# Performance work log

Measured on AMD Instinct MI355X. Metric: run time of the kernel, lower is better.

The kernel has to match this reference:

```python
import jax, jax.numpy as jnp
from jax import lax
import numpy as np

N_CLASS = 11
ROI_SIZE = 7
SPATIAL_SCALE = 1.0 / 16.0
IMG_H, IMG_W = 600, 800
SCALE = 1.0
NMS_THRESH = 0.3
SCORE_THRESH = 0.05
LOC_MEAN = (0.0, 0.0, 0.0, 0.0)
LOC_STD = (0.1, 0.1, 0.2, 0.2)


def setup_inputs() -> dict:
    key = jax.random.key(0)
    ks = jax.random.split(key, 8)
    R = 512
    h = jax.random.normal(ks[0], (1, 512, 37, 50), dtype=jnp.float32)
    u = jax.random.uniform(ks[1], (R, 4), dtype=jnp.float32)
    y1 = u[:, 0] * (IMG_H - 64.0)
    x1 = u[:, 1] * (IMG_W - 64.0)
    y2 = y1 + 32.0 + u[:, 2] * (IMG_H - y1 - 32.0)
    x2 = x1 + 32.0 + u[:, 3] * (IMG_W - x1 - 32.0)
    rois = jnp.stack([y1, x1, y2, x2], axis=1)  # (ymin,xmin,ymax,xmax)
    roi_indices = jnp.zeros((R,), dtype=jnp.int32)
    W1 = jax.random.normal(ks[2], (25088, 4096), dtype=jnp.float32) * 0.01
    b1 = jnp.zeros((4096,), dtype=jnp.float32)
    W2 = jax.random.normal(ks[3], (4096, 4096), dtype=jnp.float32) * 0.01
    b2 = jnp.zeros((4096,), dtype=jnp.float32)
    Wloc = jax.random.normal(ks[4], (4096, N_CLASS * 4), dtype=jnp.float32) * 0.001
    bloc = jnp.zeros((N_CLASS * 4,), dtype=jnp.float32)
    Wscore = jax.random.normal(ks[5], (4096, N_CLASS), dtype=jnp.float32) * 0.01
    bscore = jnp.zeros((N_CLASS,), dtype=jnp.float32)
    return {"h": h, "rois": rois, "roi_indices": roi_indices, "W1": W1, "b1": b1,
            "W2": W2, "b2": b2, "Wloc": Wloc, "bloc": bloc, "Wscore": Wscore, "bscore": bscore}


def roi_pool(feat_all, rois_xyxy, roi_indices):
    # torchvision RoIPool: quantize coords by spatial_scale (round), +1 width, floor/ceil bins, max pool
    Hf, Wf = feat_all.shape[2], feat_all.shape[3]
    ys = jnp.arange(Hf)
    xs = jnp.arange(Wf)
    pb = jnp.arange(ROI_SIZE, dtype=jnp.float32)
    neg = jnp.array(-jnp.inf, feat_all.dtype)

    def one(args):
        roi, b = args
        x1, y1, x2, y2 = roi[0], roi[1], roi[2], roi[3]
        sw = jnp.round(x1 * SPATIAL_SCALE)
        ew = jnp.round(x2 * SPATIAL_SCALE)
        sh = jnp.round(y1 * SPATIAL_SCALE)
        eh = jnp.round(y2 * SPATIAL_SCALE)
        rw = jnp.maximum(ew - sw + 1.0, 1.0)
        rh = jnp.maximum(eh - sh + 1.0, 1.0)
        hstart = jnp.clip(jnp.floor(pb * rh / ROI_SIZE) + sh, 0, Hf)
        hend = jnp.clip(jnp.ceil((pb + 1.0) * rh / ROI_SIZE) + sh, 0, Hf)
        wstart = jnp.clip(jnp.floor(pb * rw / ROI_SIZE) + sw, 0, Wf)
        wend = jnp.clip(jnp.ceil((pb + 1.0) * rw / ROI_SIZE) + sw, 0, Wf)
        mh = (ys[None, :] >= hstart[:, None]) & (ys[None, :] < hend[:, None])  # [7,Hf]
        mw = (xs[None, :] >= wstart[:, None]) & (xs[None, :] < wend[:, None])  # [7,Wf]
        feat = jnp.take(feat_all, b, axis=0)  # [C,Hf,Wf]
        rowmax = jnp.where(mh[:, None, :, None], feat[None], neg).max(axis=2)  # [7ph,C,Wf]
        binmax = jnp.where(mw[:, None, None, :], rowmax[None], neg).max(axis=3)  # [7pw,7ph,C]
        pooled = jnp.transpose(binmax, (2, 1, 0))  # [C,ph,pw]
        empty = (hend <= hstart)[:, None] | (wend <= wstart)[None, :]  # [ph,pw]
        return jnp.where(empty[None], jnp.zeros((), feat.dtype), pooled)

    return lax.map(one, (rois_xyxy, roi_indices))  # [R,C,7,7]


def loc2bbox(src, loc):
    sh = src[:, 2] - src[:, 0]
    sw = src[:, 3] - src[:, 1]
    cy = src[:, 0] + 0.5 * sh
    cx = src[:, 1] + 0.5 * sw
    ncy = loc[:, 0] * sh + cy
    ncx = loc[:, 1] * sw + cx
    nh = jnp.exp(loc[:, 2]) * sh
    nw = jnp.exp(loc[:, 3]) * sw
    return jnp.stack([ncy - 0.5 * nh, ncx - 0.5 * nw, ncy + 0.5 * nh, ncx + 0.5 * nw], axis=1)


def _forward(h, rois, roi_indices, W1, b1, W2, b2, Wloc, bloc, Wscore, bscore):
    R = rois.shape[0]
    rois_xyxy = rois[:, jnp.array([1, 0, 3, 2])]  # (x1,y1,x2,y2) for RoIPool
    pool = roi_pool(h, rois_xyxy, roi_indices).reshape(R, -1)  # [R,25088]
    fc = jax.nn.relu(pool @ W1 + b1)
    fc7 = jax.nn.relu(fc @ W2 + b2)
    roi_cls_loc = fc7 @ Wloc + bloc  # [R,44]
    roi_scores = fc7 @ Wscore + bscore  # [R,11]
    mean = jnp.tile(jnp.asarray(LOC_MEAN, jnp.float32), N_CLASS)
    std = jnp.tile(jnp.asarray(LOC_STD, jnp.float32), N_CLASS)
    roi_cls_loc = roi_cls_loc * std + mean
    roi_s = rois / SCALE
    loc3 = roi_cls_loc.reshape(-1, N_CLASS, 4)
    roi3 = jnp.broadcast_to(roi_s[:, None, :], loc3.shape)
    cls_bbox = loc2bbox(roi3.reshape(-1, 4), loc3.reshape(-1, 4)).reshape(-1, N_CLASS * 4)
    cls_bbox = cls_bbox.at[:, 0::2].set(jnp.clip(cls_bbox[:, 0::2], 0.0, IMG_H))
    cls_bbox = cls_bbox.at[:, 1::2].set(jnp.clip(cls_bbox[:, 1::2], 0.0, IMG_W))
    prob = jax.nn.softmax(roi_scores, axis=1)
    return cls_bbox, prob


def _box_iou(a, b):  # yxyx, torchvision convention (no +1)
    tl = jnp.maximum(a[:, None, :2], b[None, :, :2])
    br = jnp.minimum(a[:, None, 2:], b[None, :, 2:])
    wh = jnp.clip(br - tl, 0.0)
    inter = wh[..., 0] * wh[..., 1]
    area_a = (a[:, 2] - a[:, 0]) * (a[:, 3] - a[:, 1])
    area_b = (b[:, 2] - b[:, 0]) * (b[:, 3] - b[:, 1])
    return inter / (area_a[:, None] + area_b[None, :] - inter)


def _nms_one(boxes, scores):
    R = scores.shape[0]
    valid = scores > SCORE_THRESH
    order = jnp.argsort(jnp.where(valid, -scores, jnp.inf))
    b = boxes[order]
    v = valid[order]
    iou = _box_iou(b, b)  # [R,R]
    idx = jnp.arange(R)

    def body(i, keep):
        suppress = keep[i] & (iou[i] > NMS_THRESH) & (idx > i)
        return keep & ~suppress

    keep = lax.fori_loop(0, R, body, v)
    return jnp.zeros((R,), bool).at[order].set(keep)


def reference(h, rois, roi_indices, W1, b1, W2, b2, Wloc, bloc, Wscore, bscore):
    cls_bbox, prob = _forward(h, rois, roi_indices, W1, b1, W2, b2, Wloc, bloc, Wscore, bscore)
    R = cls_bbox.shape[0]
    boxes_c = jnp.transpose(cls_bbox.reshape(R, N_CLASS, 4)[:, 1:], (1, 0, 2))  # [10,R,4]
    scores_c = prob[:, 1:].T  # [10,R]
    keep = jax.vmap(_nms_one)(boxes_c, scores_c)  # [10,R] bool per-class keep mask
    return cls_bbox, prob, keep
```

## Files before the change

### kernel.cpp

```cpp
#include <hip/hip_runtime.h>
#include <cfloat>
#include <cmath>
#include <stdint.h>

#define R_ROIS 512
#define NCLS 11
#define FEAT_C 512
#define FEAT_H 37
#define FEAT_W 50
#define POOLSZ 7
#define POOL_DIM (FEAT_C * POOLSZ * POOLSZ)
#define FC_DIM 4096
#define IMG_Hf 600.0f
#define IMG_Wf 800.0f
#define SPATIAL_SCALE 0.0625f
#define NMS_THR 0.3f
#define SCORE_THR 0.05f

#define OUT_PROB_OFF (R_ROIS * NCLS * 4)
#define OUT_KEEP_OFF (OUT_PROB_OFF + R_ROIS * NCLS)

typedef __bf16 bf16;
typedef __attribute__((ext_vector_type(8))) __bf16 v8bf;
typedef __attribute__((ext_vector_type(4))) __bf16 v4bf;
typedef __attribute__((ext_vector_type(4))) float f32x4;
typedef unsigned int u32;

__device__ __forceinline__ void gload_lds16(const void* g, void* l) {
  __builtin_amdgcn_global_load_lds(
      (const __attribute__((address_space(1))) u32*)(uintptr_t)g,
      (__attribute__((address_space(3))) u32*)(uintptr_t)l, 16, 0, 0);
}

__global__ __launch_bounds__(256) void roi_pool_kernel(
    const float* __restrict__ feat, const float* __restrict__ rois,
    const int* __restrict__ roi_idx, bf16* __restrict__ pool) {
  int r = blockIdx.x;
  float y1 = rois[r * 4 + 0], x1 = rois[r * 4 + 1];
  float y2 = rois[r * 4 + 2], x2 = rois[r * 4 + 3];
  float sw = rintf(x1 * SPATIAL_SCALE), ew = rintf(x2 * SPATIAL_SCALE);
  float sh = rintf(y1 * SPATIAL_SCALE), eh = rintf(y2 * SPATIAL_SCALE);
  float rw = fmaxf(ew - sw + 1.0f, 1.0f);
  float rh = fmaxf(eh - sh + 1.0f, 1.0f);
  int hs[POOLSZ], he[POOLSZ], wsA[POOLSZ], weA[POOLSZ];
#pragma unroll
  for (int p = 0; p < POOLSZ; ++p) {
    float fp = (float)p;
    hs[p] = (int)fminf(fmaxf(floorf(fp * rh / 7.0f) + sh, 0.0f), (float)FEAT_H);
    he[p] = (int)fminf(fmaxf(ceilf((fp + 1.0f) * rh / 7.0f) + sh, 0.0f), (float)FEAT_H);
    wsA[p] = (int)fminf(fmaxf(floorf(fp * rw / 7.0f) + sw, 0.0f), (float)FEAT_W);
    weA[p] = (int)fminf(fmaxf(ceilf((fp + 1.0f) * rw / 7.0f) + sw, 0.0f), (float)FEAT_W);
  }
  const float* f = feat + (size_t)roi_idx[r] * FEAT_C * FEAT_H * FEAT_W;
  for (int idx = threadIdx.x; idx < POOL_DIM; idx += 256) {
    int c = idx / 49;
    int rem = idx - c * 49;
    int p = rem / 7;
    int q = rem - p * 7;
    float v = 0.0f;
    if (he[p] > hs[p] && weA[q] > wsA[q]) {
      v = -FLT_MAX;
      const float* fc = f + (size_t)c * FEAT_H * FEAT_W;
      for (int y = hs[p]; y < he[p]; ++y)
        for (int x = wsA[q]; x < weA[q]; ++x)
          v = fmaxf(v, fc[y * FEAT_W + x]);
    }
    pool[(size_t)r * POOL_DIM + idx] = (bf16)v;
  }
}

__global__ __launch_bounds__(256) void whead_transpose(
    const float* __restrict__ Wloc, const float* __restrict__ Wscore,
    float* __restrict__ WT) {
  int o = blockIdx.x;
  for (int k = threadIdx.x; k < FC_DIM; k += 256) {
    float v = (o < 44) ? Wloc[(size_t)k * 44 + o]
                       : Wscore[(size_t)k * 11 + (o - 44)];
    WT[(size_t)o * FC_DIM + k] = v;
  }
}

__global__ __launch_bounds__(256) void gemm_mfma(
    const bf16* __restrict__ A, const float* __restrict__ B,
    float* __restrict__ part, int K, int Kper) {
  __shared__ __align__(16) bf16 As[128 * 32];
  __shared__ __align__(16) bf16 Bs[128 * 40];
  int tid = threadIdx.x;
  int bm = blockIdx.x * 128;
  int bn = blockIdx.y * 128;
  int s = blockIdx.z;
  int kbeg = s * Kper;
  int kend = kbeg + Kper;
  int lane = tid & 63;
  int wave = tid >> 6;
  int wm = (wave >> 1) * 64;
  int wn = (wave & 1) * 64;

  f32x4 acc[4][4];
#pragma unroll
  for (int i = 0; i < 4; ++i)
#pragma unroll
    for (int j = 0; j < 4; ++j) acc[i][j] = (f32x4){0.f, 0.f, 0.f, 0.f};

  int arow = tid >> 2;
  int acol = (tid & 3) * 8;
  const bf16* Ag0 = A + (size_t)(bm + arow) * K + acol;
  const bf16* Ag1 = A + (size_t)(bm + 64 + arow) * K + acol;
  bf16* Ad0 = As + tid * 8;
  bf16* Ad1 = As + 2048 + tid * 8;

  int nB = tid & 127;
  int khB = (tid >> 7) * 16;
  const float* Bg = B + (size_t)khB * FC_DIM + bn + nB;
  bf16* Bd = Bs + nB * 40 + khB;

  for (int k0 = kbeg; k0 < kend; k0 += 32) {
    __syncthreads();
    gload_lds16(Ag0 + k0, Ad0);
    gload_lds16(Ag1 + k0, Ad1);
    const float* bp = Bg + (size_t)k0 * FC_DIM;
    float bv[16];
#pragma unroll
    for (int j = 0; j < 16; ++j) bv[j] = bp[(size_t)j * FC_DIM];
    v8bf blo, bhi;
#pragma unroll
    for (int j = 0; j < 8; ++j) blo[j] = (bf16)bv[j];
#pragma unroll
    for (int j = 0; j < 8; ++j) bhi[j] = (bf16)bv[8 + j];
    *(v8bf*)(Bd) = blo;
    *(v8bf*)(Bd + 8) = bhi;
    __syncthreads();

    v8bf af[4], bfr[4];
#pragma unroll
    for (int i = 0; i < 4; ++i)
      af[i] = *(const v8bf*)(As + (wm + i * 16 + (lane & 15)) * 32 +
                             (lane >> 4) * 8);
#pragma unroll
    for (int j = 0; j < 4; ++j)
      bfr[j] = *(const v8bf*)(Bs + (wn + j * 16 + (lane & 15)) * 40 +
                              (lane >> 4) * 8);
#pragma unroll
    for (int i = 0; i < 4; ++i)
#pragma unroll
      for (int j = 0; j < 4; ++j)
        acc[i][j] = __builtin_amdgcn_mfma_f32_16x16x32_bf16(af[i], bfr[j],
                                                            acc[i][j], 0, 0, 0);
  }

  int cn = lane & 15;
  int rq = (lane >> 4) * 4;
  float* po = part + ((size_t)s * R_ROIS + bm + wm + rq) * FC_DIM + bn + wn + cn;
#pragma unroll
  for (int i = 0; i < 4; ++i)
#pragma unroll
    for (int r = 0; r < 4; ++r) {
      float* pr = po + (size_t)(i * 16 + r) * FC_DIM;
#pragma unroll
      for (int j = 0; j < 4; ++j) pr[j * 16] = acc[i][j][r];
    }
}

__global__ __launch_bounds__(256) void reduce_bias_relu(
    const float* __restrict__ part, const float* __restrict__ bias, int S,
    bf16* __restrict__ out_bf, float* __restrict__ out_f32) {
  int idx = (blockIdx.x * 256 + threadIdx.x) * 4;
  f32x4 sum = *(const f32x4*)(part + idx);
  for (int s = 1; s < S; ++s)
    sum += *(const f32x4*)(part + (size_t)s * R_ROIS * FC_DIM + idx);
  int n = idx & (FC_DIM - 1);
  f32x4 b = *(const f32x4*)(bias + n);
  sum += b;
#pragma unroll
  for (int c = 0; c < 4; ++c) sum[c] = fmaxf(sum[c], 0.0f);
  *(f32x4*)(out_f32 + idx) = sum;
  v4bf h;
#pragma unroll
  for (int c = 0; c < 4; ++c) h[c] = (bf16)sum[c];
  *(v4bf*)(out_bf + idx) = h;
}

__global__ __launch_bounds__(256) void head_kernel(
    const float* __restrict__ fc7, const float* __restrict__ WT,
    const float* __restrict__ bloc, const float* __restrict__ bscore,
    const float* __restrict__ rois, float* __restrict__ out) {
  __shared__ float row[FC_DIM];
  __shared__ float outv[64];
  int r = blockIdx.x;
  int tid = threadIdx.x;
  for (int k = tid * 4; k < FC_DIM; k += 1024)
    *(float4*)(row + k) = *(const float4*)(fc7 + (size_t)r * FC_DIM + k);
  __syncthreads();
  int wave = tid >> 6, lane = tid & 63;
  for (int o = wave; o < 55; o += 4) {
    const float* w = WT + (size_t)o * FC_DIM;
    float p = 0.0f;
    for (int k = lane * 4; k < FC_DIM; k += 256) {
      float4 a = *(const float4*)(row + k);
      float4 b = *(const float4*)(w + k);
      p += a.x * b.x + a.y * b.y + a.z * b.z + a.w * b.w;
    }
#pragma unroll
    for (int off = 32; off; off >>= 1) p += __shfl_down(p, off);
    if (lane == 0) outv[o] = p;
  }
  __syncthreads();
  if (tid == 0) {
    float sarr[NCLS];
    float m = -FLT_MAX;
#pragma unroll
    for (int j = 0; j < NCLS; ++j) {
      sarr[j] = outv[44 + j] + bscore[j];
      m = fmaxf(m, sarr[j]);
    }
    float sum = 0.0f;
#pragma unroll
    for (int j = 0; j < NCLS; ++j) {
      sarr[j] = expf(sarr[j] - m);
      sum += sarr[j];
    }
    float inv = 1.0f / sum;
#pragma unroll
    for (int j = 0; j < NCLS; ++j)
      out[OUT_PROB_OFF + r * NCLS + j] = sarr[j] * inv;
    float y1 = rois[r * 4 + 0], x1 = rois[r * 4 + 1];
    float y2 = rois[r * 4 + 2], x2 = rois[r * 4 + 3];
    float shh = y2 - y1, sww = x2 - x1;
    float cy = y1 + 0.5f * shh, cx = x1 + 0.5f * sww;
    const float STD[4] = {0.1f, 0.1f, 0.2f, 0.2f};
    for (int c = 0; c < NCLS; ++c) {
      float l0 = (outv[c * 4 + 0] + bloc[c * 4 + 0]) * STD[0];
      float l1 = (outv[c * 4 + 1] + bloc[c * 4 + 1]) * STD[1];
      float l2 = (outv[c * 4 + 2] + bloc[c * 4 + 2]) * STD[2];
      float l3 = (outv[c * 4 + 3] + bloc[c * 4 + 3]) * STD[3];
      float ncy = l0 * shh + cy, ncx = l1 * sww + cx;
      float nh = expf(l2) * shh, nw = expf(l3) * sww;
      out[r * 44 + c * 4 + 0] = fminf(fmaxf(ncy - 0.5f * nh, 0.0f), IMG_Hf);
      out[r * 44 + c * 4 + 1] = fminf(fmaxf(ncx - 0.5f * nw, 0.0f), IMG_Wf);
      out[r * 44 + c * 4 + 2] = fminf(fmaxf(ncy + 0.5f * nh, 0.0f), IMG_Hf);
      out[r * 44 + c * 4 + 3] = fminf(fmaxf(ncx + 0.5f * nw, 0.0f), IMG_Wf);
    }
  }
}

__device__ __forceinline__ bool key_lt(float ka, int ia, float kb, int ib) {
  return (ka < kb) || (ka == kb && ia < ib);
}

__global__ __launch_bounds__(512) void nms_kernel(
    const float* __restrict__ cls_bbox, const float* __restrict__ prob,
    float* __restrict__ keep_out) {
  int c = blockIdx.x + 1;
  int tid = threadIdx.x;
  __shared__ float skey[512];
  __shared__ int sidx[512];
  __shared__ float by1[512], bx1[512], by2[512], bx2[512], sarea[512];
  __shared__ int skeep[512];
  float s = prob[tid * NCLS + c];
  skey[tid] = (s > SCORE_THR) ? -s : INFINITY;
  sidx[tid] = tid;
  for (int k = 2; k <= 512; k <<= 1) {
    for (int j = k >> 1; j > 0; j >>= 1) {
      __syncthreads();
      int ixj = tid ^ j;
      if (ixj > tid) {
        float k1 = skey[tid], k2 = skey[ixj];
        int i1 = sidx[tid], i2 = sidx[ixj];
        bool up = ((tid & k) == 0);
        bool do_swap = up ? key_lt(k2, i2, k1, i1) : key_lt(k1, i1, k2, i2);
        if (do_swap) {
          skey[tid] = k2; skey[ixj] = k1;
          sidx[tid] = i2; sidx[ixj] = i1;
        }
      }
    }
  }
  __syncthreads();
  {
    int r = sidx[tid];
    float yy1 = cls_bbox[r * 44 + c * 4 + 0];
    float xx1 = cls_bbox[r * 44 + c * 4 + 1];
    float yy2 = cls_bbox[r * 44 + c * 4 + 2];
    float xx2 = cls_bbox[r * 44 + c * 4 + 3];
    by1[tid] = yy1; bx1[tid] = xx1; by2[tid] = yy2; bx2[tid] = xx2;
    sarea[tid] = (yy2 - yy1) * (xx2 - xx1);
    skeep[tid] = (skey[tid] != INFINITY) ? 1 : 0;
  }
  for (int i = 0; i < 511; ++i) {
    __syncthreads();
    if (!skeep[i]) continue;
    int j = tid;
    if (j > i && skeep[j]) {
      float ty = fmaxf(by1[i], by1[j]);
      float tx = fmaxf(bx1[i], bx1[j]);
      float byy = fminf(by2[i], by2[j]);
      float bxx = fminf(bx2[i], bx2[j]);
      float hh = fmaxf(byy - ty, 0.0f);
      float ww = fmaxf(bxx - tx, 0.0f);
      float inter = hh * ww;
      float iou = inter / (sarea[i] + sarea[j] - inter);
      if (iou > NMS_THR) skeep[j] = 0;
    }
  }
  __syncthreads();
  keep_out[(size_t)(c - 1) * R_ROIS + sidx[tid]] = skeep[tid] ? 1.0f : 0.0f;
}

extern "C" void kernel_launch(void* const* d_in, const int* in_sizes, int n_in,
                              void* d_out, int out_size, void* d_ws,
                              size_t ws_size, hipStream_t stream) {
  const float* h = (const float*)d_in[0];
  const float* rois = (const float*)d_in[1];
  const int* roi_indices = (const int*)d_in[2];
  const float* W1 = (const float*)d_in[3];
  const float* b1 = (const float*)d_in[4];
  const float* W2 = (const float*)d_in[5];
  const float* b2 = (const float*)d_in[6];
  const float* Wloc = (const float*)d_in[7];
  const float* bloc = (const float*)d_in[8];
  const float* Wscore = (const float*)d_in[9];
  const float* bscore = (const float*)d_in[10];
  float* out = (float*)d_out;

  char* ws = (char*)d_ws;
  size_t off = 0;
  bf16* pool_bf = (bf16*)(ws + off); off += (size_t)R_ROIS * POOL_DIM * 2;
  bf16* fc_bf = (bf16*)(ws + off);   off += (size_t)R_ROIS * FC_DIM * 2;
  float* fc7 = (float*)(ws + off);   off += (size_t)R_ROIS * FC_DIM * 4;
  float* WT = (float*)(ws + off);    off += (size_t)55 * FC_DIM * 4;
  float* part = (float*)(ws + off);
  size_t part_bytes_per_s = (size_t)R_ROIS * FC_DIM * 4;
  int S = (ws_size - off >= 4 * part_bytes_per_s) ? 4 : 2;

  roi_pool_kernel<<<R_ROIS, 256, 0, stream>>>(h, rois, roi_indices, pool_bf);
  whead_transpose<<<55, 256, 0, stream>>>(Wloc, Wscore, WT);

  gemm_mfma<<<dim3(4, 32, S), 256, 0, stream>>>(pool_bf, W1, part, POOL_DIM,
                                                POOL_DIM / S);
  reduce_bias_relu<<<(R_ROIS * FC_DIM) / 1024, 256, 0, stream>>>(
      part, b1, S, fc_bf, fc7 );

  gemm_mfma<<<dim3(4, 32, S), 256, 0, stream>>>(fc_bf, W2, part, FC_DIM,
                                                FC_DIM / S);
  reduce_bias_relu<<<(R_ROIS * FC_DIM) / 1024, 256, 0, stream>>>(
      part, b2, S, fc_bf , fc7);

  head_kernel<<<R_ROIS, 256, 0, stream>>>(fc7, WT, bloc, bscore, rois, out);
  nms_kernel<<<10, 512, 0, stream>>>(out, out + OUT_PROB_OFF,
                                     out + OUT_KEEP_OFF);
}
```

Baseline: 1.497 ms.

## Transpose feature map to HWC bf16 and pool channel pairs with LDS staging

Adds a pre-pass that converts the CHW fp32 feature map into an HWC bf16 layout. RoI pooling then has each thread handle two adjacent channels per 32-bit load, so loads are coalesced across channels. Pooled values are staged in LDS and written out with 16-byte vector stores in the original C-major order. Doing the max in bf16 keeps the result the same, since rounding is monotonic, but it adds one extra kernel launch and a small transpose pass. An unused truncating variant of the transpose kernel is also left in the file.

After: 1.221 ms. 18.4% less time.

```diff
diff --git a/kernel.cpp b/kernel.cpp
--- a/kernel.cpp
+++ b/kernel.cpp
@@ -8,6 +8,7 @@
 #define FEAT_C 512
 #define FEAT_H 37
 #define FEAT_W 50
+#define FEAT_HW (FEAT_H * FEAT_W)
 #define POOLSZ 7
 #define POOL_DIM (FEAT_C * POOLSZ * POOLSZ)
 #define FC_DIM 4096
@@ -25,6 +26,7 @@
 typedef __attribute__((ext_vector_type(4))) __bf16 v4bf;
 typedef __attribute__((ext_vector_type(4))) float f32x4;
 typedef unsigned int u32;
+typedef unsigned short u16;
 
 __device__ __forceinline__ void gload_lds16(const void* g, void* l) {
   __builtin_amdgcn_global_load_lds(
@@ -32,10 +34,28 @@
       (__attribute__((address_space(3))) u32*)(uintptr_t)l, 16, 0, 0);
 }
 
-__global__ __launch_bounds__(256) void roi_pool_kernel(
-    const float* __restrict__ feat, const float* __restrict__ rois,
+__global__ __launch_bounds__(512) void feat_transpose(
+    const float* __restrict__ feat, u16* __restrict__ featT) {
+  int yx = blockIdx.x;
+  int c = threadIdx.x;
+  float v = feat[(size_t)c * FEAT_HW + yx];
+  featT[(size_t)yx * FEAT_C + c] = (u16)(__float_as_uint(v) >> 16) ;
+}
+__global__ __launch_bounds__(512) void feat_transpose_rne(
+    const float* __restrict__ feat, u16* __restrict__ featT) {
+  int yx = blockIdx.x;
+  int c = threadIdx.x;
+  float v = feat[(size_t)c * FEAT_HW + yx];
+  bf16 b = (bf16)v;
+  featT[(size_t)yx * FEAT_C + c] = *(u16*)&b;
+}
+
+__global__ __launch_bounds__(256) void roi_pool_hwc(
+    const u16* __restrict__ featT, const float* __restrict__ rois,
     const int* __restrict__ roi_idx, bf16* __restrict__ pool) {
+  __shared__ u16 lds[POOL_DIM];
   int r = blockIdx.x;
+  int tid = threadIdx.x;
   float y1 = rois[r * 4 + 0], x1 = rois[r * 4 + 1];
   float y2 = rois[r * 4 + 2], x2 = rois[r * 4 + 3];
   float sw = rintf(x1 * SPATIAL_SCALE), ew = rintf(x2 * SPATIAL_SCALE);
@@ -51,22 +71,36 @@
     wsA[p] = (int)fminf(fmaxf(floorf(fp * rw / 7.0f) + sw, 0.0f), (float)FEAT_W);
     weA[p] = (int)fminf(fmaxf(ceilf((fp + 1.0f) * rw / 7.0f) + sw, 0.0f), (float)FEAT_W);
   }
-  const float* f = feat + (size_t)roi_idx[r] * FEAT_C * FEAT_H * FEAT_W;
-  for (int idx = threadIdx.x; idx < POOL_DIM; idx += 256) {
-    int c = idx / 49;
-    int rem = idx - c * 49;
-    int p = rem / 7;
-    int q = rem - p * 7;
-    float v = 0.0f;
-    if (he[p] > hs[p] && weA[q] > wsA[q]) {
-      v = -FLT_MAX;
-      const float* fc = f + (size_t)c * FEAT_H * FEAT_W;
-      for (int y = hs[p]; y < he[p]; ++y)
-        for (int x = wsA[q]; x < weA[q]; ++x)
-          v = fmaxf(v, fc[y * FEAT_W + x]);
-    }
-    pool[(size_t)r * POOL_DIM + idx] = (bf16)v;
-  }
+  const u32* fb = (const u32*)(featT + (size_t)roi_idx[r] * FEAT_HW * FEAT_C) + tid;
+#pragma unroll
+  for (int p = 0; p < POOLSZ; ++p) {
+    int h0 = hs[p], h1 = he[p];
+#pragma unroll
+    for (int q = 0; q < POOLSZ; ++q) {
+      int w0 = wsA[q], w1 = weA[q];
+      float m0, m1;
+      if (h1 > h0 && w1 > w0) {
+        m0 = -FLT_MAX; m1 = -FLT_MAX;
+        for (int y = h0; y < h1; ++y) {
+          const u32* row = fb + ((size_t)(y * FEAT_W) << 8);
+          for (int x = w0; x < w1; ++x) {
+            u32 u = row[(size_t)x << 8];
+            m0 = fmaxf(m0, __uint_as_float(u << 16));
+            m1 = fmaxf(m1, __uint_as_float(u & 0xffff0000u));
+          }
+        }
+      } else {
+        m0 = 0.0f; m1 = 0.0f;
+      }
+      int bin = p * 7 + q;
+      lds[(2 * tid) * 49 + bin] = (u16)(__float_as_uint(m0) >> 16);
+      lds[(2 * tid + 1) * 49 + bin] = (u16)(__float_as_uint(m1) >> 16);
+    }
+  }
+  __syncthreads();
+  bf16* po = pool + (size_t)r * POOL_DIM;
+  for (int idx = tid * 8; idx < POOL_DIM; idx += 2048)
+    *(v8bf*)(po + idx) = *(const v8bf*)(lds + idx);
 }
 
 __global__ __launch_bounds__(256) void whead_transpose(
@@ -328,22 +362,24 @@
   bf16* fc_bf = (bf16*)(ws + off);   off += (size_t)R_ROIS * FC_DIM * 2;
   float* fc7 = (float*)(ws + off);   off += (size_t)R_ROIS * FC_DIM * 4;
   float* WT = (float*)(ws + off);    off += (size_t)55 * FC_DIM * 4;
+  u16* featT = (u16*)(ws + off);     off += (size_t)FEAT_HW * FEAT_C * 2;
   float* part = (float*)(ws + off);
   size_t part_bytes_per_s = (size_t)R_ROIS * FC_DIM * 4;
   int S = (ws_size - off >= 4 * part_bytes_per_s) ? 4 : 2;
 
-  roi_pool_kernel<<<R_ROIS, 256, 0, stream>>>(h, rois, roi_indices, pool_bf);
+  feat_transpose_rne<<<FEAT_HW, 512, 0, stream>>>(h, featT);
   whead_transpose<<<55, 256, 0, stream>>>(Wloc, Wscore, WT);
+  roi_pool_hwc<<<R_ROIS, 256, 0, stream>>>(featT, rois, roi_indices, pool_bf);
 
   gemm_mfma<<<dim3(4, 32, S), 256, 0, stream>>>(pool_bf, W1, part, POOL_DIM,
                                                 POOL_DIM / S);
   reduce_bias_relu<<<(R_ROIS * FC_DIM) / 1024, 256, 0, stream>>>(
-      part, b1, S, fc_bf, fc7 );
+      part, b1, S, fc_bf, fc7);
 
   gemm_mfma<<<dim3(4, 32, S), 256, 0, stream>>>(fc_bf, W2, part, FC_DIM,
                                                 FC_DIM / S);
   reduce_bias_relu<<<(R_ROIS * FC_DIM) / 1024, 256, 0, stream>>>(
-      part, b2, S, fc_bf , fc7);
+      part, b2, S, fc_bf, fc7);
 
   head_kernel<<<R_ROIS, 256, 0, stream>>>(fc7, WT, bloc, bscore, rois, out);
   nms_kernel<<<10, 512, 0, stream>>>(out, out + OUT_PROB_OFF,
```
